# Kernel tuning notes

Hardware: AMD Instinct MI355X
Metric: run time of the kernel (lower is better)

Reference implementation:

```python
import jax, jax.numpy as jnp
import numpy as np


def gcn_conv(h, W, b, src, dst):
    # PyG GCNConv: h @ W, add self-loops, symmetric deg^-1/2 normalization,
    # scatter-add messages from src to dst, then add bias.
    n = h.shape[0]
    h = h @ W                                   # [N, out]
    loop = jnp.arange(n, dtype=src.dtype)
    row = jnp.concatenate([src, loop])          # message sources
    col = jnp.concatenate([dst, loop])          # aggregation targets
    deg = jax.ops.segment_sum(jnp.ones_like(col, dtype=h.dtype), col, num_segments=n)
    dinv = jnp.where(deg > 0, jax.lax.rsqrt(deg), 0.0)
    norm = dinv[row] * dinv[col]                # [E+N]
    out = jax.ops.segment_sum(h[row] * norm[:, None], col, num_segments=n)
    return out + b


def setup_inputs() -> dict:
    key = jax.random.key(0)
    ks = jax.random.split(key, 12)
    N, E = 50000, 800000
    in_dim, hid, out_dim = 768, 256, 128
    x = jax.random.normal(ks[0], (N, in_dim), dtype=jnp.float32)
    edge_index = jax.random.randint(ks[1], (2, E), 0, N, dtype=jnp.int64)

    def lin(k, fan_in, fan_out):
        bound = 1.0 / np.sqrt(fan_in)
        kw, kb = jax.random.split(k)
        W = jax.random.uniform(kw, (fan_in, fan_out), jnp.float32, -bound, bound)
        b = jax.random.uniform(kb, (fan_out,), jnp.float32, -bound, bound)
        return W, b

    W1, b1 = lin(ks[2], in_dim, hid)
    Wg1, bg1 = lin(ks[3], hid, hid)
    Wg2, bg2 = lin(ks[4], hid, hid)
    W2, b2 = lin(ks[5], hid, out_dim)
    Wc, bc = lin(ks[6], out_dim, 2)
    return {
        "x": x, "edge_index": edge_index,
        "W1": W1, "b1": b1, "Wg1": Wg1, "bg1": bg1,
        "Wg2": Wg2, "bg2": bg2, "W2": W2, "b2": b2,
        "Wc": Wc, "bc": bc, "batch_size": 1024,
    }


def reference(x, edge_index, W1, b1, Wg1, bg1, Wg2, bg2, W2, b2, Wc, bc, batch_size):
    src, dst = edge_index[0], edge_index[1]
    h = jax.nn.relu(x @ W1 + b1)                # linear_relu1
    h = gcn_conv(h, Wg1, bg1, src, dst)         # text1
    # dropout is identity in eval mode
    h = gcn_conv(h, Wg2, bg2, src, dst)         # text2
    h = jax.nn.relu(h @ W2 + b2)                # linear_relu2
    logits = h @ Wc + bc                        # classifier
    return logits[:batch_size]
```

## Files before the change

### kernel.cpp

```cpp
#include <hip/hip_runtime.h>
#include <hip/hip_bf16.h>
#include <cstdint>
#include <cstddef>
#include <type_traits>

typedef _Float16 half8 __attribute__((ext_vector_type(8)));
typedef _Float16 half4v __attribute__((ext_vector_type(4)));
typedef float float4v __attribute__((ext_vector_type(4)));


__global__ void k_zero2(int* __restrict__ a, int* __restrict__ b, int n) {
  int i = blockIdx.x * blockDim.x + threadIdx.x;
  if (i < n) { a[i] = 0; b[i] = 0; }
}

__global__ void k_count(const int* __restrict__ dst, int* __restrict__ cnt, int E) {
  int e = blockIdx.x * blockDim.x + threadIdx.x;
  if (e < E) atomicAdd(&cnt[dst[e]], 1);
}

__global__ void k_mark(const int* __restrict__ src, const int* __restrict__ dst,
                       int* __restrict__ flag, int E, int Batch) {
  int e = blockIdx.x * blockDim.x + threadIdx.x;
  if (e < E && dst[e] < Batch) flag[src[e]] = 1;
  if (e < Batch) flag[e] = 1;
}

__global__ __launch_bounds__(1024) void k_scan_local(const int* __restrict__ cnt,
                                                     int* __restrict__ rowp,
                                                     int* __restrict__ bsum, int n) {
  __shared__ int sm[1024];
  int tid = threadIdx.x;
  int i = blockIdx.x * 1024 + tid;
  int v = (i < n) ? cnt[i] : 0;
  sm[tid] = v;
  __syncthreads();
  for (int off = 1; off < 1024; off <<= 1) {
    int t = (tid >= off) ? sm[tid - off] : 0;
    __syncthreads();
    sm[tid] += t;
    __syncthreads();
  }
  if (i < n) rowp[i] = sm[tid] - v;
  if (tid == 1023) bsum[blockIdx.x] = sm[1023];
}

__global__ __launch_bounds__(1024) void k_scan_sums(int* __restrict__ bsum, int nb) {
  __shared__ int sm[1024];
  int tid = threadIdx.x;
  int v = (tid < nb) ? bsum[tid] : 0;
  sm[tid] = v;
  __syncthreads();
  for (int off = 1; off < 1024; off <<= 1) {
    int t = (tid >= off) ? sm[tid - off] : 0;
    __syncthreads();
    sm[tid] += t;
    __syncthreads();
  }
  if (tid < nb) bsum[tid] = sm[tid] - v;
}

__global__ void k_finalize(int* __restrict__ rowp, const int* __restrict__ bsum,
                           const int* __restrict__ cnt, int* __restrict__ cursor,
                           float* __restrict__ dinv, int n, int E) {
  int i = blockIdx.x * blockDim.x + threadIdx.x;
  if (i < n) {
    int v = rowp[i] + bsum[i >> 10];
    rowp[i] = v;
    cursor[i] = v;
    dinv[i] = rsqrtf((float)(cnt[i] + 1));
  }
  if (i == 0) rowp[n] = E;
}

__global__ void k_fill(const int* __restrict__ src, const int* __restrict__ dst,
                       int* __restrict__ cursor, int* __restrict__ csr_src, int E) {
  int e = blockIdx.x * blockDim.x + threadIdx.x;
  if (e < E) {
    int pos = atomicAdd(&cursor[dst[e]], 1);
    csr_src[pos] = src[e];
  }
}

__global__ void k_emit(const int* __restrict__ flag, const int* __restrict__ fidx,
                       const int* __restrict__ fbsum, int* __restrict__ list,
                       int* __restrict__ s1cnt, int n) {
  int i = blockIdx.x * blockDim.x + threadIdx.x;
  if (i >= n) return;
  int pos = fidx[i] + fbsum[i >> 10];
  if (flag[i]) list[pos] = i;
  if (i == n - 1) s1cnt[0] = pos + flag[i];
}


__global__ void k_w_convert_all(const float* __restrict__ W1, const float* __restrict__ Wg1,
                                const float* __restrict__ Wg2, _Float16* __restrict__ W1t,
                                _Float16* __restrict__ Wg1t, _Float16* __restrict__ Wg2t,
                                int in_dim, int hid) {
  int idx = blockIdx.x * blockDim.x + threadIdx.x;
  int n1 = in_dim * hid;
  int n2 = hid * hid;
  if (idx < n1) {
    int n = idx / in_dim, k = idx - n * in_dim;
    W1t[idx] = (_Float16)W1[(size_t)k * hid + n];
  } else if (idx < n1 + n2) {
    int i2 = idx - n1;
    int n = i2 / hid, k = i2 - n * hid;
    Wg1t[i2] = (_Float16)Wg1[(size_t)k * hid + n];
  } else if (idx < n1 + 2 * n2) {
    int i2 = idx - n1 - n2;
    int n = i2 / hid, k = i2 - n * hid;
    Wg2t[i2] = (_Float16)Wg2[(size_t)k * hid + n];
  }
}


__device__ __forceinline__ void gl_lds16(const void* g, void* l) {
  __builtin_amdgcn_global_load_lds(
      (const __attribute__((address_space(1))) void*)g,
      (__attribute__((address_space(3))) void*)l, 16, 0, 0);
}

#define VMCNT(n) asm volatile("s_waitcnt vmcnt(" #n ")" ::: "memory")

template <int RA>
__device__ __forceinline__ void dma_tile(const char* const (&aS)[RA], const int (&aD)[RA],
                                         const char* const (&bS)[2], const int (&bD)[2],
                                         char* ab, char* bb, size_t advA, size_t advB) {
#pragma unroll
  for (int rr = 0; rr < RA; ++rr) gl_lds16(aS[rr] + advA, ab + aD[rr]);
#pragma unroll
  for (int rr = 0; rr < 2; ++rr) gl_lds16(bS[rr] + advB, bb + bD[rr]);
}

template <typename AT, int RELU, int BIAS, int SCALE, int GATHER>
__global__ __launch_bounds__(512) void k_gemm_mfma(const AT* __restrict__ A,
                                                   const _Float16* __restrict__ Bt,
                                                   const float* __restrict__ bias,
                                                   const float* __restrict__ rowscale,
                                                   _Float16* __restrict__ out,
                                                   int M, int N, int K,
                                                   const int* __restrict__ ridx,
                                                   const int* __restrict__ rcnt) {
  __shared__ alignas(16) AT Asm[3][256 * 32];
  __shared__ alignas(16) _Float16 Bsm[3][256 * 32];
  constexpr bool AF32 = std::is_same_v<AT, float>;
  constexpr int RA = AF32 ? 4 : 2;
  constexpr int ABUFB = 256 * 32 * (int)sizeof(AT);
  constexpr int BBUFB = 256 * 32 * 2;

  const int tid = threadIdx.x;
  const int wv = tid >> 6;
  const int ln = tid & 63;
  const int quad = ln >> 4;
  const int l15 = ln & 15;
  const int wm = (wv >> 2) * 128;
  const int wn = (wv & 3) * 64;

  const int bm = (int)blockIdx.x * 256;

  int Meff = M;
  if constexpr (GATHER) {
    Meff = rcnt[0];
    if (bm >= Meff) return;
  }

  const char* aSrcB[RA];
  int aDstOff[RA];
#pragma unroll
  for (int rr = 0; rr < RA; ++rr) {
    int q = rr * 8192 + wv * 1024 + ln * 16;
    int row, colE;
    if constexpr (AF32) {
      int h = q >> 14;
      row = (q >> 6) & 255;
      colE = ((q & 63) >> 2) + (h << 4);
    } else {
      row = q >> 6;
      colE = (q & 63) >> 1;
    }
    int li = bm + row; if (li > Meff - 1) li = Meff - 1;
    int grow;
    if constexpr (GATHER) grow = ridx[li]; else grow = li;
    aSrcB[rr] = (const char*)(A + (size_t)grow * K + colE);
    aDstOff[rr] = rr * 8192 + wv * 1024;
  }
  const char* bSrcB[2];
  int bDstOff[2];
#pragma unroll
  for (int rr = 0; rr < 2; ++rr) {
    int q = rr * 8192 + wv * 1024 + ln * 16;
    int row = q >> 6;
    int colH = (q & 63) >> 1;
    bSrcB[rr] = (const char*)(Bt + (size_t)row * K + colH);
    bDstOff[rr] = rr * 8192 + wv * 1024;
  }

  float4v acc[8][4];
#pragma unroll
  for (int i = 0; i < 8; ++i)
#pragma unroll
    for (int j = 0; j < 4; ++j) acc[i][j] = (float4v){0.f, 0.f, 0.f, 0.f};

  const int nk = K >> 5;

  char* const Ab0 = (char*)&Asm[0][0];
  char* const Bb0 = (char*)&Bsm[0][0];

  dma_tile<RA>(aSrcB, aDstOff, bSrcB, bDstOff, Ab0, Bb0, 0, 0);
  dma_tile<RA>(aSrcB, aDstOff, bSrcB, bDstOff, Ab0 + ABUFB, Bb0 + BBUFB,
               (size_t)32 * sizeof(AT), 64);

  int c0 = 0;
  for (int kt = 0; kt < nk; ++kt) {
    if (kt + 1 < nk) {
      if constexpr (AF32) { VMCNT(6); } else { VMCNT(4); }
    } else {
      VMCNT(0);
    }
    __builtin_amdgcn_sched_barrier(0);
    __builtin_amdgcn_s_barrier();
    __builtin_amdgcn_sched_barrier(0);

    if (kt + 2 < nk) {
      int c2 = c0 + 2; if (c2 >= 3) c2 -= 3;
      dma_tile<RA>(aSrcB, aDstOff, bSrcB, bDstOff,
                   Ab0 + (size_t)c2 * ABUFB, Bb0 + (size_t)c2 * BBUFB,
                   (size_t)(kt + 2) * 32 * sizeof(AT), (size_t)(kt + 2) * 64);
      __builtin_amdgcn_sched_barrier(0);
    }

    const AT* Ab = &Asm[c0][0];
    const _Float16* Bb = &Bsm[c0][0];
    half8 bf[4];
#pragma unroll
    for (int j = 0; j < 4; ++j)
      bf[j] = *(const half8*)(Bb + (wn + j * 16 + l15) * 32 + quad * 8);
#pragma unroll
    for (int i = 0; i < 8; ++i) {
      int rowa = wm + i * 16 + l15;
      half8 af;
      if constexpr (AF32) {
        const float* ap = Ab + (quad >> 1) * 4096 + rowa * 16 + (quad & 1) * 8;
        float4v f0 = *(const float4v*)ap;
        float4v f1 = *(const float4v*)(ap + 4);
        af[0] = (_Float16)f0[0]; af[1] = (_Float16)f0[1];
        af[2] = (_Float16)f0[2]; af[3] = (_Float16)f0[3];
        af[4] = (_Float16)f1[0]; af[5] = (_Float16)f1[1];
        af[6] = (_Float16)f1[2]; af[7] = (_Float16)f1[3];
      } else {
        af = *(const half8*)(Ab + rowa * 32 + quad * 8);
      }
#pragma unroll
      for (int j = 0; j < 4; ++j)
        acc[i][j] = __builtin_amdgcn_mfma_f32_16x16x32_f16(af, bf[j], acc[i][j], 0, 0, 0);
    }

    c0 = (c0 == 2) ? 0 : c0 + 1;
  }

#pragma unroll
  for (int j = 0; j < 4; ++j) {
    int c = wn + j * 16 + l15;
    float bv = BIAS ? bias[c] : 0.f;
#pragma unroll
    for (int i = 0; i < 8; ++i) {
      int rbase = bm + wm + i * 16 + quad * 4;
      float4v a = acc[i][j];
#pragma unroll
      for (int reg = 0; reg < 4; ++reg) {
        int r = rbase + reg;
        if (r < Meff) {
          int orow;
          if constexpr (GATHER) orow = ridx[r]; else orow = r;
          float v = a[reg] + bv;
          if (RELU) v = fmaxf(v, 0.f);
          if (SCALE) v *= rowscale[orow];
          out[(size_t)orow * N + c] = (_Float16)v;
        }
      }
    }
  }
}


template <int RELU, int BIAS>
__global__ __launch_bounds__(256) void k_gemm(const float* __restrict__ A,
                                              const float* __restrict__ B,
                                              const float* __restrict__ bias,
                                              float* __restrict__ C,
                                              int M, int N, int K) {
  __shared__ float As[16][68];
  __shared__ float Bs[16][68];
  const int bm = blockIdx.y * 64;
  const int bn = blockIdx.x * 64;
  const int tid = threadIdx.x;
  const int tr = (tid >> 4) << 2;
  const int tc = (tid & 15) << 2;
  const int lm  = tid >> 2;
  const int lk  = (tid & 3) << 2;
  const int lk2 = tid >> 4;
  const int ln  = (tid & 15) << 2;
  const bool arow_ok = (bm + lm) < M;
  const float* Aptr = A + (size_t)(bm + lm) * K + lk;
  const float* Bptr = B + (size_t)lk2 * N + bn + ln;
  float acc[4][4] = {};
  for (int k0 = 0; k0 < K; k0 += 16) {
    float4 a4 = make_float4(0.f, 0.f, 0.f, 0.f);
    if (arow_ok) a4 = *(const float4*)(Aptr + k0);
    float4 b4 = *(const float4*)(Bptr + (size_t)k0 * N);
    As[lk + 0][lm] = a4.x;
    As[lk + 1][lm] = a4.y;
    As[lk + 2][lm] = a4.z;
    As[lk + 3][lm] = a4.w;
    *(float4*)&Bs[lk2][ln] = b4;
    __syncthreads();
#pragma unroll
    for (int k = 0; k < 16; ++k) {
      float4 av = *(const float4*)&As[k][tr];
      float4 bv = *(const float4*)&Bs[k][tc];
      float a[4] = {av.x, av.y, av.z, av.w};
      float b[4] = {bv.x, bv.y, bv.z, bv.w};
#pragma unroll
      for (int i = 0; i < 4; ++i)
#pragma unroll
        for (int j = 0; j < 4; ++j) acc[i][j] += a[i] * b[j];
    }
    __syncthreads();
  }
  float bias_v[4] = {0.f, 0.f, 0.f, 0.f};
  if (BIAS) {
    float4 bb = *(const float4*)(bias + bn + tc);
    bias_v[0] = bb.x; bias_v[1] = bb.y; bias_v[2] = bb.z; bias_v[3] = bb.w;
  }
#pragma unroll
  for (int i = 0; i < 4; ++i) {
    int r = bm + tr + i;
    if (r < M) {
      float4 o;
      o.x = acc[i][0] + bias_v[0];
      o.y = acc[i][1] + bias_v[1];
      o.z = acc[i][2] + bias_v[2];
      o.w = acc[i][3] + bias_v[3];
      if (RELU) {
        o.x = fmaxf(o.x, 0.f); o.y = fmaxf(o.y, 0.f);
        o.z = fmaxf(o.z, 0.f); o.w = fmaxf(o.w, 0.f);
      }
      *(float4*)&C[(size_t)r * N + bn + tc] = o;
    }
  }
}


template <typename OT>
__global__ __launch_bounds__(256) void k_agg(const _Float16* __restrict__ t,
                                             const int* __restrict__ row_ptr,
                                             const int* __restrict__ csr_src,
                                             const float* __restrict__ dinv,
                                             const float* __restrict__ bias,
                                             OT* __restrict__ out, int n_nodes) {
  int w = (int)((blockIdx.x * 256 + threadIdx.x) >> 6);
  int lane = threadIdx.x & 63;
  if (w >= n_nodes) return;
  float di = dinv[w];
  half4v v = *(const half4v*)(t + (size_t)w * 256 + lane * 4);
  float ax = (float)v[0], ay = (float)v[1], az = (float)v[2], aw = (float)v[3];
  int e0 = row_ptr[w], e1 = row_ptr[w + 1];
  int e = e0;
  for (; e + 4 <= e1; e += 4) {
    int s0 = csr_src[e];
    int s1 = csr_src[e + 1];
    int s2 = csr_src[e + 2];
    int s3 = csr_src[e + 3];
    half4v u0 = *(const half4v*)(t + (size_t)s0 * 256 + lane * 4);
    half4v u1 = *(const half4v*)(t + (size_t)s1 * 256 + lane * 4);
    half4v u2 = *(const half4v*)(t + (size_t)s2 * 256 + lane * 4);
    half4v u3 = *(const half4v*)(t + (size_t)s3 * 256 + lane * 4);
    ax += (float)u0[0] + (float)u1[0] + (float)u2[0] + (float)u3[0];
    ay += (float)u0[1] + (float)u1[1] + (float)u2[1] + (float)u3[1];
    az += (float)u0[2] + (float)u1[2] + (float)u2[2] + (float)u3[2];
    aw += (float)u0[3] + (float)u1[3] + (float)u2[3] + (float)u3[3];
  }
  for (; e < e1; ++e) {
    int s = csr_src[e];
    half4v u = *(const half4v*)(t + (size_t)s * 256 + lane * 4);
    ax += (float)u[0]; ay += (float)u[1]; az += (float)u[2]; aw += (float)u[3];
  }
  const float4 b = ((const float4*)bias)[lane];
  if constexpr (std::is_same_v<OT, float>) {
    float4 o;
    o.x = ax * di + b.x; o.y = ay * di + b.y;
    o.z = az * di + b.z; o.w = aw * di + b.w;
    ((float4*)(out + (size_t)w * 256))[lane] = o;
  } else {
    half4v o;
    o[0] = (_Float16)(ax * di + b.x); o[1] = (_Float16)(ay * di + b.y);
    o[2] = (_Float16)(az * di + b.z); o[3] = (_Float16)(aw * di + b.w);
    *(half4v*)(out + (size_t)w * 256 + lane * 4) = o;
  }
}

__global__ __launch_bounds__(256) void k_agg_g(const _Float16* __restrict__ t,
                                               const int* __restrict__ row_ptr,
                                               const int* __restrict__ csr_src,
                                               const float* __restrict__ dinv,
                                               const float* __restrict__ bias,
                                               _Float16* __restrict__ out,
                                               const int* __restrict__ list,
                                               const int* __restrict__ s1cnt) {
  int wi = (int)((blockIdx.x * 256 + threadIdx.x) >> 6);
  int lane = threadIdx.x & 63;
  if (wi >= s1cnt[0]) return;
  int w = list[wi];
  float di = dinv[w];
  half4v v = *(const half4v*)(t + (size_t)w * 256 + lane * 4);
  float ax = (float)v[0], ay = (float)v[1], az = (float)v[2], aw = (float)v[3];
  int e0 = row_ptr[w], e1 = row_ptr[w + 1];
  int e = e0;
  for (; e + 4 <= e1; e += 4) {
    int s0 = csr_src[e];
    int s1 = csr_src[e + 1];
    int s2 = csr_src[e + 2];
    int s3 = csr_src[e + 3];
    half4v u0 = *(const half4v*)(t + (size_t)s0 * 256 + lane * 4);
    half4v u1 = *(const half4v*)(t + (size_t)s1 * 256 + lane * 4);
    half4v u2 = *(const half4v*)(t + (size_t)s2 * 256 + lane * 4);
    half4v u3 = *(const half4v*)(t + (size_t)s3 * 256 + lane * 4);
    ax += (float)u0[0] + (float)u1[0] + (float)u2[0] + (float)u3[0];
    ay += (float)u0[1] + (float)u1[1] + (float)u2[1] + (float)u3[1];
    az += (float)u0[2] + (float)u1[2] + (float)u2[2] + (float)u3[2];
    aw += (float)u0[3] + (float)u1[3] + (float)u2[3] + (float)u3[3];
  }
  for (; e < e1; ++e) {
    int s = csr_src[e];
    half4v u = *(const half4v*)(t + (size_t)s * 256 + lane * 4);
    ax += (float)u[0]; ay += (float)u[1]; az += (float)u[2]; aw += (float)u[3];
  }
  const float4 b = ((const float4*)bias)[lane];
  half4v o;
  o[0] = (_Float16)(ax * di + b.x); o[1] = (_Float16)(ay * di + b.y);
  o[2] = (_Float16)(az * di + b.z); o[3] = (_Float16)(aw * di + b.w);
  *(half4v*)(out + (size_t)w * 256 + lane * 4) = o;
}


__global__ __launch_bounds__(256) void k_cls(const float* __restrict__ h,
                                             const float* __restrict__ Wc,
                                             const float* __restrict__ bc,
                                             float* __restrict__ out, int M, int K) {
  __shared__ float w[512];
  for (int i = threadIdx.x; i < 2 * K; i += 256) w[i] = Wc[i];
  __syncthreads();
  int i = blockIdx.x * 256 + threadIdx.x;
  if (i >= M) return;
  float a0 = bc[0], a1 = bc[1];
  const float* hr = h + (size_t)i * K;
  for (int k = 0; k < K; ++k) {
    float a = hr[k];
    a0 += a * w[2 * k];
    a1 += a * w[2 * k + 1];
  }
  out[2 * i] = a0;
  out[2 * i + 1] = a1;
}


extern "C" void kernel_launch(void* const* d_in, const int* in_sizes, int n_in,
                              void* d_out, int out_size, void* d_ws, size_t ws_size,
                              hipStream_t stream) {
  const float* x   = (const float*)d_in[0];
  const int*   ei  = (const int*)d_in[1];
  const float* W1  = (const float*)d_in[2];
  const float* b1  = (const float*)d_in[3];
  const float* Wg1 = (const float*)d_in[4];
  const float* bg1 = (const float*)d_in[5];
  const float* Wg2 = (const float*)d_in[6];
  const float* bg2 = (const float*)d_in[7];
  const float* W2  = (const float*)d_in[8];
  const float* b2  = (const float*)d_in[9];
  const float* Wc  = (const float*)d_in[10];
  const float* bc  = (const float*)d_in[11];
  float* out = (float*)d_out;

  const int hid     = in_sizes[3];
  const int in_dim  = in_sizes[2] / hid;
  const int out_dim = in_sizes[9];
  const int N       = in_sizes[0] / in_dim;
  const int E       = in_sizes[1] / 2;
  const int Batch   = out_size / 2;

  const int* srcI = ei;
  const int* dstI = ei + E;

  char* ws = (char*)d_ws;
  size_t off = 0;
  auto alloc = [&](size_t bytes) -> void* {
    void* p = ws + off;
    off = (off + bytes + 255) & ~(size_t)255;
    return p;
  };
  _Float16* h0h  = (_Float16*)alloc((size_t)N * hid * 2);
  _Float16* t1h  = (_Float16*)alloc((size_t)N * hid * 2);
  _Float16* h1h  = (_Float16*)alloc((size_t)N * hid * 2);
  _Float16* t2h  = (_Float16*)alloc((size_t)N * hid * 2);
  _Float16* W1t  = (_Float16*)alloc((size_t)in_dim * hid * 2);
  _Float16* Wg1t = (_Float16*)alloc((size_t)hid * hid * 2);
  _Float16* Wg2t = (_Float16*)alloc((size_t)hid * hid * 2);
  float* agg2    = (float*)alloc((size_t)Batch * hid * 4);
  float* h3      = (float*)alloc((size_t)Batch * out_dim * 4);
  float* dinv    = (float*)alloc((size_t)N * 4);
  int*   cnt     = (int*)alloc((size_t)N * 4);
  int*   rowp    = (int*)alloc((size_t)(N + 1) * 4);
  int*   bsum    = (int*)alloc((size_t)1024 * 4);
  int*   cursor  = (int*)alloc((size_t)N * 4);
  int*   csrs    = (int*)alloc((size_t)E * 4);
  int*   flag    = (int*)alloc((size_t)N * 4);
  int*   fidx    = (int*)alloc((size_t)N * 4);
  int*   list    = (int*)alloc((size_t)N * 4);
  int*   s1cnt   = (int*)alloc((size_t)64);
  (void)ws_size; (void)n_in;

  dim3 blk(256);
  const int nb = (N + 1023) / 1024;

  k_zero2<<<(N + 255) / 256, blk, 0, stream>>>(cnt, flag, N);
  k_count<<<(E + 255) / 256, blk, 0, stream>>>(dstI, cnt, E);
  k_mark<<<(E + 255) / 256, blk, 0, stream>>>(srcI, dstI, flag, E, Batch);
  k_scan_local<<<nb, 1024, 0, stream>>>(cnt, rowp, bsum, N);
  k_scan_sums<<<1, 1024, 0, stream>>>(bsum, nb);
  k_finalize<<<(N + 255) / 256, blk, 0, stream>>>(rowp, bsum, cnt, cursor, dinv, N, E);
  k_fill<<<(E + 255) / 256, blk, 0, stream>>>(srcI, dstI, cursor, csrs, E);
  k_scan_local<<<nb, 1024, 0, stream>>>(flag, fidx, bsum, N);
  k_scan_sums<<<1, 1024, 0, stream>>>(bsum, nb);
  k_emit<<<(N + 255) / 256, blk, 0, stream>>>(flag, fidx, bsum, list, s1cnt, N);

  {
    int total = in_dim * hid + 2 * hid * hid;
    k_w_convert_all<<<(total + 255) / 256, blk, 0, stream>>>(W1, Wg1, Wg2, W1t, Wg1t, Wg2t, in_dim, hid);
  }

  const int ng = (N + 255) / 256;
  dim3 gblk(512);
  k_gemm_mfma<float, 1, 1, 0, 0><<<dim3(ng), gblk, 0, stream>>>(x, W1t, b1, nullptr, h0h, N, hid, in_dim, nullptr, nullptr);
  k_gemm_mfma<_Float16, 0, 0, 1, 0><<<dim3(ng), gblk, 0, stream>>>(h0h, Wg1t, nullptr, dinv, t1h, N, hid, hid, nullptr, nullptr);
  k_agg_g<<<(N + 3) / 4, blk, 0, stream>>>(t1h, rowp, csrs, dinv, bg1, h1h, list, s1cnt);
  k_gemm_mfma<_Float16, 0, 0, 1, 1><<<dim3(ng), gblk, 0, stream>>>(h1h, Wg2t, nullptr, dinv, t2h, N, hid, hid, list, s1cnt);
  k_agg<float><<<(Batch + 3) / 4, blk, 0, stream>>>(t2h, rowp, csrs, dinv, bg2, agg2, Batch);
  k_gemm<1, 1><<<dim3(out_dim / 64, (Batch + 63) / 64), blk, 0, stream>>>(agg2, W2, b2, h3, Batch, out_dim, hid);
  k_cls<<<(Batch + 255) / 256, blk, 0, stream>>>(h3, Wc, bc, out, Batch, out_dim);
}
```

Baseline: 525.8 us.

## Fuse graph preprocessing kernels and merge final linear layers into one tail kernel

Merges zeroing with weight conversion, count with mark, and replaces the two-level scans plus finalize/emit with a single-block kernel that scans both arrays at once. It also fuses the last GEMM, ReLU and classifier into one kernel that reduces per-row partial dot products in shared memory. The aim is fewer kernel launches and fewer round trips through global memory. The cost is that the scan now runs in a single workgroup with a strided serial loop per thread, which has poor coalescing.

```diff
diff --git a/kernel.cpp b/kernel.cpp
--- a/kernel.cpp
+++ b/kernel.cpp
@@ -9,68 +9,88 @@
 typedef float float4v __attribute__((ext_vector_type(4)));
 
 
-__global__ void k_zero2(int* __restrict__ a, int* __restrict__ b, int n) {
-  int i = blockIdx.x * blockDim.x + threadIdx.x;
-  if (i < n) { a[i] = 0; b[i] = 0; }
-}
-
-__global__ void k_count(const int* __restrict__ dst, int* __restrict__ cnt, int E) {
+__global__ void k_prep(int* __restrict__ cnt, int* __restrict__ flag,
+                       const float* __restrict__ W1, const float* __restrict__ Wg1,
+                       const float* __restrict__ Wg2, _Float16* __restrict__ W1t,
+                       _Float16* __restrict__ Wg1t, _Float16* __restrict__ Wg2t,
+                       int n, int in_dim, int hid) {
+  int idx = blockIdx.x * blockDim.x + threadIdx.x;
+  if (idx < n) { cnt[idx] = 0; flag[idx] = 0; return; }
+  int w = idx - n;
+  int n1 = in_dim * hid;
+  int n2 = hid * hid;
+  if (w < n1) {
+    int nn = w / in_dim, k = w - nn * in_dim;
+    W1t[w] = (_Float16)W1[(size_t)k * hid + nn];
+  } else if (w < n1 + n2) {
+    int i2 = w - n1;
+    int nn = i2 / hid, k = i2 - nn * hid;
+    Wg1t[i2] = (_Float16)Wg1[(size_t)k * hid + nn];
+  } else if (w < n1 + 2 * n2) {
+    int i2 = w - n1 - n2;
+    int nn = i2 / hid, k = i2 - nn * hid;
+    Wg2t[i2] = (_Float16)Wg2[(size_t)k * hid + nn];
+  }
+}
+
+
+__global__ void k_countmark(const int* __restrict__ src, const int* __restrict__ dst,
+                            int* __restrict__ cnt, int* __restrict__ flag,
+                            int E, int Batch) {
   int e = blockIdx.x * blockDim.x + threadIdx.x;
-  if (e < E) atomicAdd(&cnt[dst[e]], 1);
-}
-
-__global__ void k_mark(const int* __restrict__ src, const int* __restrict__ dst,
-                       int* __restrict__ flag, int E, int Batch) {
-  int e = blockIdx.x * blockDim.x + threadIdx.x;
-  if (e < E && dst[e] < Batch) flag[src[e]] = 1;
+  if (e < E) {
+    int d = dst[e];
+    atomicAdd(&cnt[d], 1);
+    if (d < Batch) flag[src[e]] = 1;
+  }
   if (e < Batch) flag[e] = 1;
 }
 
-__global__ __launch_bounds__(1024) void k_scan_local(const int* __restrict__ cnt,
-                                                     int* __restrict__ rowp,
-                                                     int* __restrict__ bsum, int n) {
-  __shared__ int sm[1024];
-  int tid = threadIdx.x;
-  int i = blockIdx.x * 1024 + tid;
-  int v = (i < n) ? cnt[i] : 0;
-  sm[tid] = v;
+
+__global__ __launch_bounds__(1024) void k_scanall(const int* __restrict__ cnt,
+                                                  const int* __restrict__ flag,
+                                                  int* __restrict__ rowp,
+                                                  int* __restrict__ cursor,
+                                                  float* __restrict__ dinv,
+                                                  int* __restrict__ list,
+                                                  int* __restrict__ s1cnt,
+                                                  int n, int E) {
+  __shared__ int smc[1024];
+  __shared__ int smf[1024];
+  const int tid = threadIdx.x;
+  const int CPN = (n + 1023) >> 10;
+  const int base = tid * CPN;
+  int sc = 0, sf = 0;
+  for (int j = 0; j < CPN; ++j) {
+    int i = base + j;
+    if (i < n) { sc += cnt[i]; sf += flag[i]; }
+  }
+  smc[tid] = sc;
+  smf[tid] = sf;
   __syncthreads();
   for (int off = 1; off < 1024; off <<= 1) {
-    int t = (tid >= off) ? sm[tid - off] : 0;
+    int tc_ = (tid >= off) ? smc[tid - off] : 0;
+    int tf_ = (tid >= off) ? smf[tid - off] : 0;
     __syncthreads();
-    sm[tid] += t;
+    smc[tid] += tc_;
+    smf[tid] += tf_;
     __syncthreads();
   }
-  if (i < n) rowp[i] = sm[tid] - v;
-  if (tid == 1023) bsum[blockIdx.x] = sm[1023];
-}
-
-__global__ __launch_bounds__(1024) void k_scan_sums(int* __restrict__ bsum, int nb) {
-  __shared__ int sm[1024];
-  int tid = threadIdx.x;
-  int v = (tid < nb) ? bsum[tid] : 0;
-  sm[tid] = v;
-  __syncthreads();
-  for (int off = 1; off < 1024; off <<= 1) {
-    int t = (tid >= off) ? sm[tid - off] : 0;
-    __syncthreads();
-    sm[tid] += t;
-    __syncthreads();
-  }
-  if (tid < nb) bsum[tid] = sm[tid] - v;
-}
-
-__global__ void k_finalize(int* __restrict__ rowp, const int* __restrict__ bsum,
-                           const int* __restrict__ cnt, int* __restrict__ cursor,
-                           float* __restrict__ dinv, int n, int E) {
-  int i = blockIdx.x * blockDim.x + threadIdx.x;
-  if (i < n) {
-    int v = rowp[i] + bsum[i >> 10];
-    rowp[i] = v;
-    cursor[i] = v;
-    dinv[i] = rsqrtf((float)(cnt[i] + 1));
-  }
-  if (i == 0) rowp[n] = E;
+  int rc = smc[tid] - sc;
+  int rf = smf[tid] - sf;
+  for (int j = 0; j < CPN; ++j) {
+    int i = base + j;
+    if (i < n) {
+      int c = cnt[i], f = flag[i];
+      rowp[i] = rc;
+      cursor[i] = rc;
+      dinv[i] = rsqrtf((float)(c + 1));
+      if (f) list[rf] = i;
+      rc += c;
+      rf += f;
+    }
+  }
+  if (tid == 1023) { rowp[n] = E; s1cnt[0] = rf; }
 }
 
 __global__ void k_fill(const int* __restrict__ src, const int* __restrict__ dst,
@@ -79,38 +99,6 @@
   if (e < E) {
     int pos = atomicAdd(&cursor[dst[e]], 1);
     csr_src[pos] = src[e];
-  }
-}
-
-__global__ void k_emit(const int* __restrict__ flag, const int* __restrict__ fidx,
-                       const int* __restrict__ fbsum, int* __restrict__ list,
-                       int* __restrict__ s1cnt, int n) {
-  int i = blockIdx.x * blockDim.x + threadIdx.x;
-  if (i >= n) return;
-  int pos = fidx[i] + fbsum[i >> 10];
-  if (flag[i]) list[pos] = i;
-  if (i == n - 1) s1cnt[0] = pos + flag[i];
-}
-
-
-__global__ void k_w_convert_all(const float* __restrict__ W1, const float* __restrict__ Wg1,
-                                const float* __restrict__ Wg2, _Float16* __restrict__ W1t,
-                                _Float16* __restrict__ Wg1t, _Float16* __restrict__ Wg2t,
-                                int in_dim, int hid) {
-  int idx = blockIdx.x * blockDim.x + threadIdx.x;
-  int n1 = in_dim * hid;
-  int n2 = hid * hid;
-  if (idx < n1) {
-    int n = idx / in_dim, k = idx - n * in_dim;
-    W1t[idx] = (_Float16)W1[(size_t)k * hid + n];
-  } else if (idx < n1 + n2) {
-    int i2 = idx - n1;
-    int n = i2 / hid, k = i2 - n * hid;
-    Wg1t[i2] = (_Float16)Wg1[(size_t)k * hid + n];
-  } else if (idx < n1 + 2 * n2) {
-    int i2 = idx - n1 - n2;
-    int n = i2 / hid, k = i2 - n * hid;
-    Wg2t[i2] = (_Float16)Wg2[(size_t)k * hid + n];
   }
 }
 
@@ -279,74 +267,6 @@
           out[(size_t)orow * N + c] = (_Float16)v;
         }
       }
-    }
-  }
-}
-
-
-template <int RELU, int BIAS>
-__global__ __launch_bounds__(256) void k_gemm(const float* __restrict__ A,
-                                              const float* __restrict__ B,
-                                              const float* __restrict__ bias,
-                                              float* __restrict__ C,
-                                              int M, int N, int K) {
-  __shared__ float As[16][68];
-  __shared__ float Bs[16][68];
-  const int bm = blockIdx.y * 64;
-  const int bn = blockIdx.x * 64;
-  const int tid = threadIdx.x;
-  const int tr = (tid >> 4) << 2;
-  const int tc = (tid & 15) << 2;
-  const int lm  = tid >> 2;
-  const int lk  = (tid & 3) << 2;
-  const int lk2 = tid >> 4;
-  const int ln  = (tid & 15) << 2;
-  const bool arow_ok = (bm + lm) < M;
-  const float* Aptr = A + (size_t)(bm + lm) * K + lk;
-  const float* Bptr = B + (size_t)lk2 * N + bn + ln;
-  float acc[4][4] = {};
-  for (int k0 = 0; k0 < K; k0 += 16) {
-    float4 a4 = make_float4(0.f, 0.f, 0.f, 0.f);
-    if (arow_ok) a4 = *(const float4*)(Aptr + k0);
-    float4 b4 = *(const float4*)(Bptr + (size_t)k0 * N);
-    As[lk + 0][lm] = a4.x;
-    As[lk + 1][lm] = a4.y;
-    As[lk + 2][lm] = a4.z;
-    As[lk + 3][lm] = a4.w;
-    *(float4*)&Bs[lk2][ln] = b4;
-    __syncthreads();
-#pragma unroll
-    for (int k = 0; k < 16; ++k) {
-      float4 av = *(const float4*)&As[k][tr];
-      float4 bv = *(const float4*)&Bs[k][tc];
-      float a[4] = {av.x, av.y, av.z, av.w};
-      float b[4] = {bv.x, bv.y, bv.z, bv.w};
-#pragma unroll
-      for (int i = 0; i < 4; ++i)
-#pragma unroll
-        for (int j = 0; j < 4; ++j) acc[i][j] += a[i] * b[j];
-    }
-    __syncthreads();
-  }
-  float bias_v[4] = {0.f, 0.f, 0.f, 0.f};
-  if (BIAS) {
-    float4 bb = *(const float4*)(bias + bn + tc);
-    bias_v[0] = bb.x; bias_v[1] = bb.y; bias_v[2] = bb.z; bias_v[3] = bb.w;
-  }
-#pragma unroll
-  for (int i = 0; i < 4; ++i) {
-    int r = bm + tr + i;
-    if (r < M) {
-      float4 o;
-      o.x = acc[i][0] + bias_v[0];
-      o.y = acc[i][1] + bias_v[1];
-      o.z = acc[i][2] + bias_v[2];
-      o.w = acc[i][3] + bias_v[3];
-      if (RELU) {
-        o.x = fmaxf(o.x, 0.f); o.y = fmaxf(o.y, 0.f);
-        o.z = fmaxf(o.z, 0.f); o.w = fmaxf(o.w, 0.f);
-      }
-      *(float4*)&C[(size_t)r * N + bn + tc] = o;
     }
   }
 }
@@ -444,24 +364,83 @@
 }
 
 
-__global__ __launch_bounds__(256) void k_cls(const float* __restrict__ h,
-                                             const float* __restrict__ Wc,
-                                             const float* __restrict__ bc,
-                                             float* __restrict__ out, int M, int K) {
-  __shared__ float w[512];
-  for (int i = threadIdx.x; i < 2 * K; i += 256) w[i] = Wc[i];
+__global__ __launch_bounds__(256) void k_tail(const float* __restrict__ A,
+                                              const float* __restrict__ B,
+                                              const float* __restrict__ b2,
+                                              const float* __restrict__ Wc,
+                                              const float* __restrict__ bc,
+                                              float* __restrict__ out,
+                                              int M, int N, int K) {
+  __shared__ float As[16][68];
+  __shared__ float Bs[16][136];
+  __shared__ float wsm[256];
+  __shared__ float red[64][16][2];
+  const int bm = blockIdx.x * 64;
+  const int tid = threadIdx.x;
+  const int tr = (tid >> 4) << 2;
+  const int tc = (tid & 15) << 3;
+  const int lm  = tid >> 2;
+  const int lk  = (tid & 3) << 2;
+  const int lk2 = tid >> 4;
+  const int ln  = (tid & 15) << 3;
+  wsm[tid] = Wc[tid];
+  const bool arow_ok = (bm + lm) < M;
+  const float* Aptr = A + (size_t)(bm + lm) * K + lk;
+  const float* Bptr = B + (size_t)lk2 * N + ln;
+  float acc[4][8] = {};
+  for (int k0 = 0; k0 < K; k0 += 16) {
+    float4 a4 = make_float4(0.f, 0.f, 0.f, 0.f);
+    if (arow_ok) a4 = *(const float4*)(Aptr + k0);
+    float4 b4 = *(const float4*)(Bptr + (size_t)k0 * N);
+    float4 b5 = *(const float4*)(Bptr + (size_t)k0 * N + 4);
+    As[lk + 0][lm] = a4.x;
+    As[lk + 1][lm] = a4.y;
+    As[lk + 2][lm] = a4.z;
+    As[lk + 3][lm] = a4.w;
+    *(float4*)&Bs[lk2][ln] = b4;
+    *(float4*)&Bs[lk2][ln + 4] = b5;
+    __syncthreads();
+#pragma unroll
+    for (int k = 0; k < 16; ++k) {
+      float4 av = *(const float4*)&As[k][tr];
+      float a[4] = {av.x, av.y, av.z, av.w};
+      float b[8];
+      *(float4*)&b[0] = *(const float4*)&Bs[k][tc];
+      *(float4*)&b[4] = *(const float4*)&Bs[k][tc + 4];
+#pragma unroll
+      for (int i = 0; i < 4; ++i)
+#pragma unroll
+        for (int j = 0; j < 8; ++j) acc[i][j] += a[i] * b[j];
+    }
+    __syncthreads();
+  }
+  float p[4][2] = {};
+#pragma unroll
+  for (int j = 0; j < 8; ++j) {
+    float bb = b2[tc + j];
+    float w0 = wsm[(tc + j) * 2 + 0];
+    float w1 = wsm[(tc + j) * 2 + 1];
+#pragma unroll
+    for (int i = 0; i < 4; ++i) {
+      float v = fmaxf(acc[i][j] + bb, 0.f);
+      p[i][0] += v * w0;
+      p[i][1] += v * w1;
+    }
+  }
+#pragma unroll
+  for (int i = 0; i < 4; ++i) {
+    red[tr + i][tid & 15][0] = p[i][0];
+    red[tr + i][tid & 15][1] = p[i][1];
+  }
   __syncthreads();
-  int i = blockIdx.x * 256 + threadIdx.x;
-  if (i >= M) return;
-  float a0 = bc[0], a1 = bc[1];
-  const float* hr = h + (size_t)i * K;
-  for (int k = 0; k < K; ++k) {
-    float a = hr[k];
-    a0 += a * w[2 * k];
-    a1 += a * w[2 * k + 1];
-  }
-  out[2 * i] = a0;
-  out[2 * i + 1] = a1;
+  if (tid < 128) {
+    int row = tid >> 1, kk = tid & 1;
+    float s = 0.f;
+#pragma unroll
+    for (int t = 0; t < 16; ++t) s += red[row][t][kk];
+    int r = bm + row;
+    if (r < M) out[2 * r + kk] = s + bc[kk];
+  }
 }
 
 
@@ -507,37 +486,26 @@
   _Float16* Wg1t = (_Float16*)alloc((size_t)hid * hid * 2);
   _Float16* Wg2t = (_Float16*)alloc((size_t)hid * hid * 2);
   float* agg2    = (float*)alloc((size_t)Batch * hid * 4);
-  float* h3      = (float*)alloc((size_t)Batch * out_dim * 4);
   float* dinv    = (float*)alloc((size_t)N * 4);
   int*   cnt     = (int*)alloc((size_t)N * 4);
   int*   rowp    = (int*)alloc((size_t)(N + 1) * 4);
-  int*   bsum    = (int*)alloc((size_t)1024 * 4);
   int*   cursor  = (int*)alloc((size_t)N * 4);
   int*   csrs    = (int*)alloc((size_t)E * 4);
   int*   flag    = (int*)alloc((size_t)N * 4);
-  int*   fidx    = (int*)alloc((size_t)N * 4);
   int*   list    = (int*)alloc((size_t)N * 4);
   int*   s1cnt   = (int*)alloc((size_t)64);
   (void)ws_size; (void)n_in;
 
   dim3 blk(256);
-  const int nb = (N + 1023) / 1024;
-
-  k_zero2<<<(N + 255) / 256, blk, 0, stream>>>(cnt, flag, N);
-  k_count<<<(E + 255) / 256, blk, 0, stream>>>(dstI, cnt, E);
-  k_mark<<<(E + 255) / 256, blk, 0, stream>>>(srcI, dstI, flag, E, Batch);
-  k_scan_local<<<nb, 1024, 0, stream>>>(cnt, rowp, bsum, N);
-  k_scan_sums<<<1, 1024, 0, stream>>>(bsum, nb);
-  k_finalize<<<(N + 255) / 256, blk, 0, stream>>>(rowp, bsum, cnt, cursor, dinv, N, E);
+
+  {
+    int total = N + in_dim * hid + 2 * hid * hid;
+    k_prep<<<(total + 255) / 256, blk, 0, stream>>>(cnt, flag, W1, Wg1, Wg2,
+                                                    W1t, Wg1t, Wg2t, N, in_dim, hid);
+  }
+  k_countmark<<<(E + 255) / 256, blk, 0, stream>>>(srcI, dstI, cnt, flag, E, Batch);
+  k_scanall<<<1, 1024, 0, stream>>>(cnt, flag, rowp, cursor, dinv, list, s1cnt, N, E);
   k_fill<<<(E + 255) / 256, blk, 0, stream>>>(srcI, dstI, cursor, csrs, E);
-  k_scan_local<<<nb, 1024, 0, stream>>>(flag, fidx, bsum, N);
-  k_scan_sums<<<1, 1024, 0, stream>>>(bsum, nb);
-  k_emit<<<(N + 255) / 256, blk, 0, stream>>>(flag, fidx, bsum, list, s1cnt, N);
-
-  {
-    int total = in_dim * hid + 2 * hid * hid;
-    k_w_convert_all<<<(total + 255) / 256, blk, 0, stream>>>(W1, Wg1, Wg2, W1t, Wg1t, Wg2t, in_dim, hid);
-  }
 
   const int ng = (N + 255) / 256;
   dim3 gblk(512);
@@ -546,6 +514,5 @@
   k_agg_g<<<(N + 3) / 4, blk, 0, stream>>>(t1h, rowp, csrs, dinv, bg1, h1h, list, s1cnt);
   k_gemm_mfma<_Float16, 0, 0, 1, 1><<<dim3(ng), gblk, 0, stream>>>(h1h, Wg2t, nullptr, dinv, t2h, N, hid, hid, list, s1cnt);
   k_agg<float><<<(Batch + 3) / 4, blk, 0, stream>>>(t2h, rowp, csrs, dinv, bg2, agg2, Batch);
-  k_gemm<1, 1><<<dim3(out_dim / 64, (Batch + 63) / 64), blk, 0, stream>>>(agg2, W2, b2, h3, Batch, out_dim, hid);
-  k_cls<<<(Batch + 255) / 256, blk, 0, stream>>>(h3, Wc, bc, out, Batch, out_dim);
-}
+  k_tail<<<(Batch + 63) / 64, blk, 0, stream>>>(agg2, W2, b2, Wc, bc, out, Batch, out_dim, hid);
+}
```

After: 728.7 us. 1.39x slower.
